# Kernel optimization log

Hardware: AMD Instinct MI355X
Metric: run time of the kernel (lower is better)

The kernel has to match this reference:

```python
import jax, jax.numpy as jnp
import numpy as np

B, S, E, H = 2, 2048, 1024, 16
HD = E // H

def setup_inputs() -> dict:
    key = jax.random.key(0)
    ks = jax.random.split(key, 12)
    q = jax.random.normal(ks[0], (B, S, E), jnp.float32)
    k = jax.random.normal(ks[1], (B, S, E), jnp.float32)
    v = jax.random.normal(ks[2], (B, S, E), jnp.float32)
    # causal mask: 1.0 where attention is disallowed (upper triangle)
    mask = jnp.triu(jnp.ones((S, S), jnp.float32), k=1)[None, None, :, :]
    w = lambda kk: jax.random.normal(kk, (E, E), jnp.float32) * 0.02
    return {
        "q": q, "k": k, "v": v, "mask": mask,
        "Wq": w(ks[3]), "bq": jnp.zeros((E,), jnp.float32),
        "Wk": w(ks[4]), "bk": jnp.zeros((E,), jnp.float32),
        "Wv": w(ks[5]), "bv": jnp.zeros((E,), jnp.float32),
        "Wz": w(ks[6]), "bz": jnp.zeros((E,), jnp.float32),
    }

def _create_heads(x):
    # Faithful to tf.reshape(tf.transpose(x), (B, H, -1, HD)):
    # tf.transpose reverses all dims: [B,S,E] -> [E,S,B], then reshape.
    return jnp.transpose(x, (2, 1, 0)).reshape(B, H, -1, HD)

def reference(q, k, v, mask, Wq, bq, Wk, bk, Wv, bv, Wz, bz):
    qh = _create_heads(q @ Wq + bq)  # (B,H,S,HD)
    kh = _create_heads(k @ Wk + bk)
    vh = _create_heads(v @ Wv + bv)
    qn = qh / jnp.linalg.norm(qh, axis=-1, keepdims=True)
    kn = kh / jnp.linalg.norm(kh, axis=-1, keepdims=True)
    logits = jnp.einsum('bhqd,bhkd->bhqk', qn, kn) * 1000.0
    logits = logits + mask * -1000000000.0
    attn = jax.nn.softmax(logits, axis=-1)  # (B,H,S,S)
    z = jnp.einsum('bhqk,bhkd->bhqd', attn, vh)
    zc = jnp.transpose(z, (0, 2, 1, 3)).reshape(B, -1, E)
    return zc @ Wz + bz, attn
```

## Files before the change

kernel.cpp:

```cpp
#include <hip/hip_runtime.h>
#include <cstdint>
#include <cstddef>


typedef __bf16 bf16x4 __attribute__((ext_vector_type(4)));
typedef __bf16 bf16x8 __attribute__((ext_vector_type(8)));
typedef float floatx4 __attribute__((ext_vector_type(4)));

#define GLOAD_LDS16(g, l)                                                      \
    __builtin_amdgcn_global_load_lds(                                          \
        (const __attribute__((address_space(1))) void*)(g),                    \
        (__attribute__((address_space(3))) void*)(l), 16, 0, 0)

__device__ __forceinline__ void nt_store4(float* p, floatx4 v) {
    __builtin_nontemporal_store(v, (floatx4*)p);
}

__global__ __launch_bounds__(256) void prep(
    const float* __restrict__ x0, const float* __restrict__ x1,
    const float* __restrict__ x2, __bf16* __restrict__ ApBase,
    const float* __restrict__ w0, const float* __restrict__ w1,
    const float* __restrict__ w2, const float* __restrict__ w3,
    __bf16* __restrict__ Bp0, __bf16* __restrict__ BpzDst, int nW)
{
    const int flat = (int)blockIdx.x;
    const int tid = (int)threadIdx.x;

    if (flat < 12288) {
        const int z = flat >> 12;
        const int bx = flat & 4095;
        const float* X = z == 0 ? x0 : (z == 1 ? x1 : x2);
        __bf16* Ap = ApBase + (size_t)z * (4096ull * 2048);
        const int idx = bx * 256 + tid;
        const int r = idx >> 8;
        const int c = (idx & 255) * 4;
        float4 t = *(const float4*)(X + (size_t)r * 1024 + c);
        bf16x4 hi, lo;
        hi[0] = (__bf16)t.x; lo[0] = (__bf16)(t.x - (float)hi[0]);
        hi[1] = (__bf16)t.y; lo[1] = (__bf16)(t.y - (float)hi[1]);
        hi[2] = (__bf16)t.z; lo[2] = (__bf16)(t.z - (float)hi[2]);
        hi[3] = (__bf16)t.w; lo[3] = (__bf16)(t.w - (float)hi[3]);
        *(bf16x4*)(Ap + (size_t)r * 2048 + c) = hi;
        *(bf16x4*)(Ap + (size_t)r * 2048 + 1024 + c) = lo;
        return;
    }

    const int t = flat - 12288;
    const int slice = t >> 8;
    if (slice >= nW) return;
    const int idx = t & 255;
    const float* W = slice == 0 ? w0 : (slice == 1 ? w1 : (slice == 2 ? w2 : w3));
    __bf16* Bp = slice < 3 ? (Bp0 + (size_t)slice * (1024ull * 2048)) : BpzDst;

    __shared__ float tile[64][65];
    const int k0 = (idx >> 4) * 64, n0 = (idx & 15) * 64;
    #pragma unroll
    for (int p = 0; p < 4; ++p) {
        int kr = p * 16 + (tid >> 4);
        float4 v = *(const float4*)(W + (size_t)(k0 + kr) * 1024 + n0 + (tid & 15) * 4);
        tile[kr][(tid & 15) * 4 + 0] = v.x; tile[kr][(tid & 15) * 4 + 1] = v.y;
        tile[kr][(tid & 15) * 4 + 2] = v.z; tile[kr][(tid & 15) * 4 + 3] = v.w;
    }
    __syncthreads();
    const int nr = tid >> 2, kc = (tid & 3) * 16;
    bf16x8 hi0, hi1, lo0, lo1;
    #pragma unroll
    for (int j = 0; j < 8; ++j) {
        float x = tile[kc + j][nr];
        __bf16 h = (__bf16)x; hi0[j] = h; lo0[j] = (__bf16)(x - (float)h);
        float y = tile[kc + 8 + j][nr];
        __bf16 g = (__bf16)y; hi1[j] = g; lo1[j] = (__bf16)(y - (float)g);
    }
    __bf16* row = Bp + (size_t)(n0 + nr) * 2048;
    *(bf16x8*)(row + k0 + kc)            = hi0;
    *(bf16x8*)(row + k0 + kc + 8)        = hi1;
    *(bf16x8*)(row + 1024 + k0 + kc)     = lo0;
    *(bf16x8*)(row + 1024 + k0 + kc + 8) = lo1;
}

__global__ __launch_bounds__(256) void split_bt1(
    const float* __restrict__ W, __bf16* __restrict__ Bp)
{
    __shared__ float tile[64][65];
    const int tid = (int)threadIdx.x;
    const int k0 = blockIdx.y * 64, n0 = blockIdx.x * 64;
    #pragma unroll
    for (int p = 0; p < 4; ++p) {
        int kr = p * 16 + (tid >> 4);
        float4 v = *(const float4*)(W + (size_t)(k0 + kr) * 1024 + n0 + (tid & 15) * 4);
        tile[kr][(tid & 15) * 4 + 0] = v.x; tile[kr][(tid & 15) * 4 + 1] = v.y;
        tile[kr][(tid & 15) * 4 + 2] = v.z; tile[kr][(tid & 15) * 4 + 3] = v.w;
    }
    __syncthreads();
    const int nr = tid >> 2, kc = (tid & 3) * 16;
    bf16x8 hi0, hi1, lo0, lo1;
    #pragma unroll
    for (int j = 0; j < 8; ++j) {
        float x = tile[kc + j][nr];
        __bf16 h = (__bf16)x; hi0[j] = h; lo0[j] = (__bf16)(x - (float)h);
        float y = tile[kc + 8 + j][nr];
        __bf16 g = (__bf16)y; hi1[j] = g; lo1[j] = (__bf16)(y - (float)g);
    }
    __bf16* row = Bp + (size_t)(n0 + nr) * 2048;
    *(bf16x8*)(row + k0 + kc)            = hi0;
    *(bf16x8*)(row + k0 + kc + 8)        = hi1;
    *(bf16x8*)(row + 1024 + k0 + kc)     = lo0;
    *(bf16x8*)(row + 1024 + k0 + kc + 8) = lo1;
}

__global__ __launch_bounds__(256) void gemm_split(
    const __bf16* __restrict__ Ap0, size_t aSlice, int aStride,
    const __bf16* __restrict__ Bp0, size_t bSlice,
    const float* __restrict__ b0, const float* __restrict__ b1,
    const float* __restrict__ b2, float* __restrict__ Out0,
    int transposeOut, int chunksQK, int chunksV)
{
    const int z = blockIdx.z;
    const int nch = (z == 2) ? chunksV : chunksQK;
    const __bf16* Ap = Ap0 + (size_t)z * aSlice;
    const __bf16* Bp = Bp0 + (size_t)z * bSlice;
    const float* bias = z == 0 ? b0 : (z == 1 ? b1 : b2);
    float* Out = Out0 + (size_t)z * (4096ull * 1024);

    __shared__ __bf16 As[2 * 128 * 32];
    __shared__ __bf16 Bs[2 * 128 * 32];

    const int tid = (int)threadIdx.x;
    const int wave = tid >> 6, lane = tid & 63;
    const int quad = lane >> 4, tl = lane & 15;
    const int m0 = blockIdx.y * 128, n0 = blockIdx.x * 128;
    const int waveM = wave >> 1, waveN = wave & 1;

    floatx4 acc[4][4];
    #pragma unroll
    for (int i = 0; i < 4; ++i)
        #pragma unroll
        for (int j = 0; j < 4; ++j)
            acc[i][j] = (floatx4){0.f, 0.f, 0.f, 0.f};

    const int sRow  = (wave << 4) + (lane >> 2);
    const int sColB = (lane & 3) << 4;
    auto* AsL = (__attribute__((address_space(3))) char*)As;
    auto* BsL = (__attribute__((address_space(3))) char*)Bs;
    const int ldsOff = wave * 1024;

    for (int k0 = 0; k0 < 1024; k0 += 32) {
        __syncthreads();
        #pragma unroll
        for (int i = 0; i < 2; ++i) {
            GLOAD_LDS16((const char*)(Ap + (size_t)(m0 + i*64 + sRow) * aStride + k0) + sColB,
                        AsL + i * 4096 + ldsOff);
            GLOAD_LDS16((const char*)(Bp + (size_t)(n0 + i*64 + sRow) * 2048 + k0) + sColB,
                        BsL + i * 4096 + ldsOff);
            if (nch > 1) {
                GLOAD_LDS16((const char*)(Ap + 1024 + (size_t)(m0 + i*64 + sRow) * aStride + k0) + sColB,
                            AsL + 8192 + i * 4096 + ldsOff);
                GLOAD_LDS16((const char*)(Bp + 1024 + (size_t)(n0 + i*64 + sRow) * 2048 + k0) + sColB,
                            BsL + 8192 + i * 4096 + ldsOff);
            }
        }
        __syncthreads();

        bf16x8 ah[4], bh[4], al[4], bl[4];
        #pragma unroll
        for (int mt = 0; mt < 4; ++mt)
            ah[mt] = *(const bf16x8*)(As + (waveM*64 + mt*16 + tl) * 32 + quad * 8);
        #pragma unroll
        for (int nt = 0; nt < 4; ++nt)
            bh[nt] = *(const bf16x8*)(Bs + (waveN*64 + nt*16 + tl) * 32 + quad * 8);
        #pragma unroll
        for (int mt = 0; mt < 4; ++mt)
            #pragma unroll
            for (int nt = 0; nt < 4; ++nt)
                acc[mt][nt] = __builtin_amdgcn_mfma_f32_16x16x32_bf16(
                    ah[mt], bh[nt], acc[mt][nt], 0, 0, 0);
        if (nch > 1) {
            #pragma unroll
            for (int mt = 0; mt < 4; ++mt)
                al[mt] = *(const bf16x8*)(As + 4096 + (waveM*64 + mt*16 + tl) * 32 + quad * 8);
            #pragma unroll
            for (int mt = 0; mt < 4; ++mt)
                #pragma unroll
                for (int nt = 0; nt < 4; ++nt)
                    acc[mt][nt] = __builtin_amdgcn_mfma_f32_16x16x32_bf16(
                        al[mt], bh[nt], acc[mt][nt], 0, 0, 0);
        }
        if (nch > 2) {
            #pragma unroll
            for (int nt = 0; nt < 4; ++nt)
                bl[nt] = *(const bf16x8*)(Bs + 4096 + (waveN*64 + nt*16 + tl) * 32 + quad * 8);
            #pragma unroll
            for (int mt = 0; mt < 4; ++mt)
                #pragma unroll
                for (int nt = 0; nt < 4; ++nt)
                    acc[mt][nt] = __builtin_amdgcn_mfma_f32_16x16x32_bf16(
                        ah[mt], bl[nt], acc[mt][nt], 0, 0, 0);
        }
    }

    if (transposeOut) {
        #pragma unroll
        for (int nt = 0; nt < 4; ++nt) {
            const int e = n0 + waveN * 64 + nt * 16 + tl;
            const float bb = bias[e];
            #pragma unroll
            for (int mt = 0; mt < 4; ++mt) {
                floatx4 v = acc[mt][nt] + bb;
                *(floatx4*)(Out + (size_t)e * 4096 + m0 + waveM * 64 + mt * 16 + quad * 4) = v;
            }
        }
    } else {
        #pragma unroll
        for (int mt = 0; mt < 4; ++mt) {
            const int rbase = m0 + waveM * 64 + mt * 16 + quad * 4;
            #pragma unroll
            for (int nt = 0; nt < 4; ++nt) {
                const int e = n0 + waveN * 64 + nt * 16 + tl;
                const float bb = bias[e];
                #pragma unroll
                for (int reg = 0; reg < 4; ++reg)
                    Out[(size_t)(rbase + reg) * 1024 + e] = acc[mt][nt][reg] + bb;
            }
        }
    }
}

__global__ __launch_bounds__(256) void gather_all(
    const float* __restrict__ PT0, __bf16* __restrict__ Qp,
    __bf16* __restrict__ Kp, __bf16* __restrict__ Vt)
{
    const int flat = (int)blockIdx.x;
    const int tid = (int)threadIdx.x;

    if (flat < 32768) {
        const float* PT = flat < 16384 ? PT0 : (PT0 + 4194304);
        __bf16* Outp = flat < 16384 ? Qp : Kp;
        const int bx = flat & 16383;
        const int lane = tid & 63;
        const int vec  = bx * 4 + (tid >> 6);
        const int head = vec >> 11;
        const int sp   = vec & 2047;
        const int c    = (head >> 4) * 512 + (head & 15) * 32 + (sp >> 6);
        const int src  = (lane & 1) * 2048 + (sp & 63) * 32 + (lane >> 1);
        float v = PT[(size_t)c * 4096 + src];
        float ss = v * v;
        #pragma unroll
        for (int mk = 32; mk >= 1; mk >>= 1) ss += __shfl_xor(ss, mk);
        v = v / sqrtf(ss);
        __bf16 h = (__bf16)v;
        Outp[(size_t)vec * 128 + lane]      = h;
        Outp[(size_t)vec * 128 + 64 + lane] = (__bf16)(v - (float)h);
        return;
    }

    const int t = flat - 32768;
    const int st = t & 31, head = t >> 5;
    const float* PTv = PT0 + 8388608;
    const int c = (head >> 4) * 512 + (head & 15) * 32 + st;
    const float* __restrict__ row = PTv + (size_t)c * 4096;

    __shared__ float tile[64][65];
    #pragma unroll
    for (int i = 0; i < 4; ++i) {
        int o = i * 1024 + tid * 4;
        float4 v4 = *(const float4*)(row + o);
        float vals[4] = {v4.x, v4.y, v4.z, v4.w};
        #pragma unroll
        for (int e = 0; e < 4; ++e) {
            int oo = o + e;
            int d  = ((oo & 2047) & 31) * 2 + (oo >> 11);
            int sl = (oo & 2047) >> 5;
            tile[sl][d] = vals[e];
        }
    }
    __syncthreads();

    const int d = tid >> 2, jb = (tid & 3) * 16;
    bf16x8 h0, h1;
    #pragma unroll
    for (int j = 0; j < 8; ++j) {
        h0[j] = (__bf16)tile[jb + j][d];
        h1[j] = (__bf16)tile[jb + 8 + j][d];
    }
    size_t bh = ((size_t)head * 64 + d) * 2048 + st * 64 + jb;
    *(bf16x8*)(Vt + bh)     = h0;
    *(bf16x8*)(Vt + bh + 8) = h1;
}

__global__ __launch_bounds__(512, 4) void attn_mfma(
    const __bf16* __restrict__ Qp, const __bf16* __restrict__ Kp,
    const __bf16* __restrict__ Vt, float* __restrict__ Attn,
    __bf16* __restrict__ Az)
{
    const int flat = (int)blockIdx.x;
    const int head = flat & 31;
    const int idx  = flat >> 5;
    const int it   = (idx < 8) ? (15 - idx) : (idx - 8);
    const int tid = (int)threadIdx.x;
    const int w = tid >> 6, lane = tid & 63;
    const int quad = lane >> 4, tl = lane & 15;
    const int t7 = tl & 7;
    const int i0 = it * 128;
    const int jtmax = 2 * it + 1;
    const int wrowMax = i0 + w * 16 + 15;
    const int wdiag   = (i0 + w * 16) >> 6;
    const int irowBase = w * 16 + quad * 4;

    const __bf16* __restrict__ Qh = Qp + ((size_t)head * 2048 + i0) * 128;
    const __bf16* __restrict__ Kh = Kp + (size_t)head * 2048 * 128;
    const __bf16* __restrict__ Vh = Vt + (size_t)head * 64 * 2048;
    float* __restrict__ Ah = Attn + (size_t)head * ((size_t)2048 * 2048);

    __shared__ __bf16 kb[2][64 * 128];
    __shared__ __bf16 vt[2][64 * 64];
    __shared__ __bf16 ps[8][16 * 72];
    __bf16* psw = ps[w];
    auto* kbL = (__attribute__((address_space(3))) char*)&kb[0][0];
    auto* vtL = (__attribute__((address_space(3))) char*)&vt[0][0];

    const char* kSrc[2];
    #pragma unroll
    for (int i = 0; i < 2; ++i) {
        int d  = i * 512 + tid;
        int rK = d >> 4, cK = (d & 15) ^ (rK & 7);
        kSrc[i] = (const char*)(Kh + (size_t)rK * 128) + cK * 16;
    }
    const char* vSrc;
    {
        int rV = tid >> 3, cV = (tid & 7) ^ (rV & 7);
        vSrc = (const char*)(Vh + (size_t)rV * 2048) + cV * 16;
    }
    const int ok0 = ((quad)      ^ t7) * 8;
    const int ok1 = ((quad + 4)  ^ t7) * 8;
    const int ok2 = ((quad + 8)  ^ t7) * 8;
    const int ok3 = ((quad + 12) ^ t7) * 8;

    const __bf16* qrow = Qh + (size_t)(w * 16 + tl) * 128;
    bf16x8 qhi0 = *(const bf16x8*)(qrow + quad * 8);
    bf16x8 qhi1 = *(const bf16x8*)(qrow + 32 + quad * 8);
    bf16x8 qlo0 = *(const bf16x8*)(qrow + 64 + quad * 8);
    bf16x8 qlo1 = *(const bf16x8*)(qrow + 96 + quad * 8);

    for (int jt = jtmax + 1; jt < 32; ++jt) {
        floatx4 z4 = (floatx4){0.f, 0.f, 0.f, 0.f};
        #pragma unroll
        for (int g = 0; g < 4; ++g)
            nt_store4(Ah + (size_t)(i0 + w * 16 + g * 4 + quad) * 2048
                          + jt * 64 + tl * 4, z4);
    }

    float m[4], l[4];
    #pragma unroll
    for (int r = 0; r < 4; ++r) { m[r] = -3.0e38f; l[r] = 0.0f; }

    #pragma unroll
    for (int i = 0; i < 2; ++i)
        GLOAD_LDS16(kSrc[i], kbL + i * 8192 + w * 1024);

    for (int jt = 0; jt <= jtmax; ++jt) {
        const int cur = jt & 1;
        __syncthreads();
        if (jt < jtmax) {
            #pragma unroll
            for (int i = 0; i < 2; ++i)
                GLOAD_LDS16(kSrc[i] + (size_t)(jt + 1) * 16384,
                            kbL + (cur ^ 1) * 16384 + i * 8192 + w * 1024);
        }
        if (jt * 64 > wrowMax) continue;

        const __bf16* kbuf = &kb[cur][0];
        const bool diag = (jt == wdiag);
        #pragma unroll
        for (int sub = 0; sub < 4; ++sub) {
            const __bf16* kr = kbuf + (sub * 16 + tl) * 128;
            bf16x8 khi0 = *(const bf16x8*)(kr + ok0);
            bf16x8 khi1 = *(const bf16x8*)(kr + ok1);
            bf16x8 klo0 = *(const bf16x8*)(kr + ok2);
            bf16x8 klo1 = *(const bf16x8*)(kr + ok3);
            floatx4 s = (floatx4){0.f, 0.f, 0.f, 0.f};
            s = __builtin_amdgcn_mfma_f32_16x16x32_bf16(qhi0, khi0, s, 0, 0, 0);
            s = __builtin_amdgcn_mfma_f32_16x16x32_bf16(qhi1, khi1, s, 0, 0, 0);
            s = __builtin_amdgcn_mfma_f32_16x16x32_bf16(qhi0, klo0, s, 0, 0, 0);
            s = __builtin_amdgcn_mfma_f32_16x16x32_bf16(qhi1, klo1, s, 0, 0, 0);
            s = __builtin_amdgcn_mfma_f32_16x16x32_bf16(qlo0, khi0, s, 0, 0, 0);
            s = __builtin_amdgcn_mfma_f32_16x16x32_bf16(qlo1, khi1, s, 0, 0, 0);
            const int col = jt * 64 + sub * 16 + tl;
            #pragma unroll
            for (int reg = 0; reg < 4; ++reg) {
                float lv = s[reg] * 1000.0f;
                if (diag && (col > i0 + irowBase + reg)) lv = -1.0e9f;
                float mn = fmaxf(m[reg], lv);
                l[reg] = l[reg] * __expf(m[reg] - mn) + __expf(lv - mn);
                m[reg] = mn;
            }
        }
    }

    #pragma unroll
    for (int reg = 0; reg < 4; ++reg) {
        #pragma unroll
        for (int mk = 8; mk >= 1; mk >>= 1) {
            float mo = __shfl_xor(m[reg], mk);
            float lo = __shfl_xor(l[reg], mk);
            float mn = fmaxf(m[reg], mo);
            l[reg] = l[reg] * __expf(m[reg] - mn) + lo * __expf(mo - mn);
            m[reg] = mn;
        }
    }
    float inv_l[4];
    #pragma unroll
    for (int reg = 0; reg < 4; ++reg) inv_l[reg] = 1.0f / l[reg];

    floatx4 zacc[4];
    #pragma unroll
    for (int t = 0; t < 4; ++t) zacc[t] = (floatx4){0.f, 0.f, 0.f, 0.f};

    #pragma unroll
    for (int i = 0; i < 2; ++i)
        GLOAD_LDS16(kSrc[i], kbL + i * 8192 + w * 1024);
    GLOAD_LDS16(vSrc, vtL + w * 1024);

    for (int jt = 0; jt <= jtmax; ++jt) {
        const int cur = jt & 1;
        __syncthreads();
        if (jt < jtmax) {
            #pragma unroll
            for (int i = 0; i < 2; ++i)
                GLOAD_LDS16(kSrc[i] + (size_t)(jt + 1) * 16384,
                            kbL + (cur ^ 1) * 16384 + i * 8192 + w * 1024);
            GLOAD_LDS16(vSrc + (size_t)(jt + 1) * 128,
                        vtL + (cur ^ 1) * 8192 + w * 1024);
        }

        if (jt * 64 > wrowMax) {
            floatx4 z4 = (floatx4){0.f, 0.f, 0.f, 0.f};
            #pragma unroll
            for (int g = 0; g < 4; ++g)
                nt_store4(Ah + (size_t)(i0 + w * 16 + g * 4 + quad) * 2048
                              + jt * 64 + tl * 4, z4);
            continue;
        }

        const __bf16* kbuf = &kb[cur][0];
        const __bf16* vbuf = &vt[cur][0];
        const bool diag = (jt == wdiag);
        #pragma unroll
        for (int sub = 0; sub < 4; ++sub) {
            const __bf16* kr = kbuf + (sub * 16 + tl) * 128;
            bf16x8 khi0 = *(const bf16x8*)(kr + ok0);
            bf16x8 khi1 = *(const bf16x8*)(kr + ok1);
            bf16x8 klo0 = *(const bf16x8*)(kr + ok2);
            bf16x8 klo1 = *(const bf16x8*)(kr + ok3);
            floatx4 s = (floatx4){0.f, 0.f, 0.f, 0.f};
            s = __builtin_amdgcn_mfma_f32_16x16x32_bf16(qhi0, khi0, s, 0, 0, 0);
            s = __builtin_amdgcn_mfma_f32_16x16x32_bf16(qhi1, khi1, s, 0, 0, 0);
            s = __builtin_amdgcn_mfma_f32_16x16x32_bf16(qhi0, klo0, s, 0, 0, 0);
            s = __builtin_amdgcn_mfma_f32_16x16x32_bf16(qhi1, klo1, s, 0, 0, 0);
            s = __builtin_amdgcn_mfma_f32_16x16x32_bf16(qlo0, khi0, s, 0, 0, 0);
            s = __builtin_amdgcn_mfma_f32_16x16x32_bf16(qlo1, khi1, s, 0, 0, 0);
            const int col = jt * 64 + sub * 16 + tl;
            #pragma unroll
            for (int reg = 0; reg < 4; ++reg) {
                float lv = s[reg] * 1000.0f;
                if (diag && (col > i0 + irowBase + reg)) lv = -1.0e9f;
                float p = __expf(lv - m[reg]) * inv_l[reg];
                psw[(quad * 4 + reg) * 72 + sub * 16 + tl] = (__bf16)p;
            }
        }
        __asm__ volatile("s_waitcnt lgkmcnt(0)" ::: "memory");

        #pragma unroll
        for (int g = 0; g < 4; ++g) {
            bf16x4 pv = *(const bf16x4*)(psw + (g * 4 + quad) * 72 + tl * 4);
            floatx4 f = (floatx4){(float)pv[0], (float)pv[1],
                                  (float)pv[2], (float)pv[3]};
            nt_store4(Ah + (size_t)(i0 + w * 16 + g * 4 + quad) * 2048
                          + jt * 64 + tl * 4, f);
        }

        bf16x8 p0 = *(const bf16x8*)(psw + tl * 72 + quad * 8);
        bf16x8 p1 = *(const bf16x8*)(psw + tl * 72 + 32 + quad * 8);
        #pragma unroll
        for (int t = 0; t < 4; ++t) {
            const __bf16* vh0 = vbuf + (t * 16 + tl) * 64;
            bf16x8 vhi0 = *(const bf16x8*)(vh0 + ok0);
            bf16x8 vhi1 = *(const bf16x8*)(vh0 + ok1);
            zacc[t] = __builtin_amdgcn_mfma_f32_16x16x32_bf16(p0, vhi0, zacc[t], 0, 0, 0);
            zacc[t] = __builtin_amdgcn_mfma_f32_16x16x32_bf16(p1, vhi1, zacc[t], 0, 0, 0);
        }
    }

    const int b = head >> 4, h = head & 15;
    #pragma unroll
    for (int reg = 0; reg < 4; ++reg) {
        const size_t R = (size_t)b * 2048 + i0 + w * 16 + quad * 4 + reg;
        #pragma unroll
        for (int t = 0; t < 4; ++t)
            Az[R * 1024 + h * 64 + t * 16 + tl] = (__bf16)zacc[t][reg];
    }
}

extern "C" void kernel_launch(void* const* d_in, const int* in_sizes, int n_in,
                              void* d_out, int out_size, void* d_ws, size_t ws_size,
                              hipStream_t stream) {
    (void)in_sizes; (void)n_in; (void)out_size;
    const float* q  = (const float*)d_in[0];
    const float* k  = (const float*)d_in[1];
    const float* v  = (const float*)d_in[2];
    const float* Wq = (const float*)d_in[4];  const float* bq = (const float*)d_in[5];
    const float* Wk = (const float*)d_in[6];  const float* bk = (const float*)d_in[7];
    const float* Wv = (const float*)d_in[8];  const float* bv = (const float*)d_in[9];
    const float* Wz = (const float*)d_in[10]; const float* bz = (const float*)d_in[11];

    float* out0 = (float*)d_out;
    float* attn = out0 + 4194304;

    float*  PT0 = attn;
    __bf16* Ap0 = (__bf16*)(attn + 12582912);
    __bf16* Bp0 = (__bf16*)(attn + 12582912 + 12582912);

    __bf16 *Qp, *Kp, *Vtp, *Az, *Bpz;
    const bool bigWs = ws_size >= (size_t)54525952;
    if (bigWs) {
        __bf16* ws = (__bf16*)d_ws;
        Qp = ws; Kp = ws + 8388608; Vtp = ws + 16777216; Az = ws + 20971520;
        Bpz = ws + 25165824;
    } else {
        Qp = (__bf16*)d_in[0]; Kp = (__bf16*)d_in[1]; Vtp = (__bf16*)d_in[2];
        Az = (__bf16*)d_ws;
        Bpz = (__bf16*)d_in[4];
    }

    if (bigWs) {
        prep<<<dim3(12288 + 4 * 256), 256, 0, stream>>>(
            q, k, v, Ap0, Wq, Wk, Wv, Wz, Bp0, Bpz, 4);
    } else {
        prep<<<dim3(12288 + 3 * 256), 256, 0, stream>>>(
            q, k, v, Ap0, Wq, Wk, Wv, Wz, Bp0, nullptr, 3);
        split_bt1<<<dim3(16, 16), 256, 0, stream>>>(Wz, Bpz);
    }

    gemm_split<<<dim3(8, 32, 3), 256, 0, stream>>>(
        Ap0, 4096ull*2048, 2048, Bp0, 1024ull*2048,
        bq, bk, bv, PT0, 1, 3, 1);

    gather_all<<<dim3(33792), 256, 0, stream>>>(PT0, Qp, Kp, Vtp);

    attn_mfma<<<dim3(512), 512, 0, stream>>>(Qp, Kp, Vtp, attn, Az);

    gemm_split<<<dim3(8, 32, 1), 256, 0, stream>>>(
        Az, 0, 1024, Bpz, 0,
        bz, bz, bz, out0, 0, 1, 1);
}
```

Baseline: 806.1 us.

## Fuse Q/K head reshaping and L2 normalization into projection GEMM epilogue

The Q and K projection GEMM blocks now remap their A-row loads so each wave's output tile holds whole head vectors. The epilogue adds bias, computes the L2 norm with a cross-lane shuffle, and writes the normalized hi/lo bf16 split directly into the per-head layout. This removes the fp32 transposed round-trip through PT0 and the separate gather pass for Q and K, leaving a smaller kernel that only transposes V. The cost is scattered 2-byte stores in the epilogue and extra registers in the GEMM.

```diff
diff --git a/kernel.cpp b/kernel.cpp
--- a/kernel.cpp
+++ b/kernel.cpp
@@ -113,10 +113,12 @@
     const __bf16* __restrict__ Bp0, size_t bSlice,
     const float* __restrict__ b0, const float* __restrict__ b1,
     const float* __restrict__ b2, float* __restrict__ Out0,
-    int transposeOut, int chunksQK, int chunksV)
+    int transposeOut, int chunksQK, int chunksV,
+    __bf16* __restrict__ Qp, __bf16* __restrict__ Kp, int fuseQK)
 {
     const int z = blockIdx.z;
     const int nch = (z == 2) ? chunksV : chunksQK;
+    const bool fuse = fuseQK && (z < 2);
     const __bf16* Ap = Ap0 + (size_t)z * aSlice;
     const __bf16* Bp = Bp0 + (size_t)z * bSlice;
     const float* bias = z == 0 ? b0 : (z == 1 ? b1 : b2);
@@ -144,16 +146,28 @@
     auto* BsL = (__attribute__((address_space(3))) char*)Bs;
     const int ldsOff = wave * 1024;
 
+    size_t aRow[2];
+    #pragma unroll
+    for (int i = 0; i < 2; ++i) {
+        const int mrow = i * 64 + sRow;
+        if (fuse) {
+            const int u = mrow & 63;
+            aRow[i] = (size_t)((u >> 5) * 2048 + (m0 >> 1) + (mrow >> 6) * 32 + (u & 31));
+        } else {
+            aRow[i] = (size_t)(m0 + mrow);
+        }
+    }
+
     for (int k0 = 0; k0 < 1024; k0 += 32) {
         __syncthreads();
         #pragma unroll
         for (int i = 0; i < 2; ++i) {
-            GLOAD_LDS16((const char*)(Ap + (size_t)(m0 + i*64 + sRow) * aStride + k0) + sColB,
+            GLOAD_LDS16((const char*)(Ap + aRow[i] * aStride + k0) + sColB,
                         AsL + i * 4096 + ldsOff);
             GLOAD_LDS16((const char*)(Bp + (size_t)(n0 + i*64 + sRow) * 2048 + k0) + sColB,
                         BsL + i * 4096 + ldsOff);
             if (nch > 1) {
-                GLOAD_LDS16((const char*)(Ap + 1024 + (size_t)(m0 + i*64 + sRow) * aStride + k0) + sColB,
+                GLOAD_LDS16((const char*)(Ap + 1024 + aRow[i] * aStride + k0) + sColB,
                             AsL + 8192 + i * 4096 + ldsOff);
                 GLOAD_LDS16((const char*)(Bp + 1024 + (size_t)(n0 + i*64 + sRow) * 2048 + k0) + sColB,
                             BsL + 8192 + i * 4096 + ldsOff);
@@ -198,7 +212,42 @@
         }
     }
 
-    if (transposeOut) {
+    if (fuse) {
+        __bf16* Outp = (z == 0) ? Qp : Kp;
+        const int g = ((m0 >> 7) << 1) + waveM;
+        #pragma unroll
+        for (int nt = 0; nt < 4; ++nt) {
+            const int e = n0 + waveN * 64 + nt * 16 + tl;
+            const float bb = bias[e];
+            float vals[16];
+            float ss = 0.f;
+            #pragma unroll
+            for (int mt = 0; mt < 4; ++mt)
+                #pragma unroll
+                for (int reg = 0; reg < 4; ++reg) {
+                    float vv = acc[mt][nt][reg] + bb;
+                    vals[mt * 4 + reg] = vv;
+                    ss += vv * vv;
+                }
+            ss += __shfl_xor(ss, 16);
+            ss += __shfl_xor(ss, 32);
+            const float inv = 1.0f / sqrtf(ss);
+            const int head = ((e >> 9) << 4) + ((e >> 5) & 15);
+            const int sp = ((e & 31) << 6) + g;
+            __bf16* row = Outp + ((size_t)head * 2048 + sp) * 128;
+            #pragma unroll
+            for (int mt = 0; mt < 4; ++mt)
+                #pragma unroll
+                for (int reg = 0; reg < 4; ++reg) {
+                    const int u = mt * 16 + quad * 4 + reg;
+                    const int d = ((u & 31) << 1) | (u >> 5);
+                    float vv = vals[mt * 4 + reg] * inv;
+                    __bf16 h = (__bf16)vv;
+                    row[d] = h;
+                    row[64 + d] = (__bf16)(vv - (float)h);
+                }
+        }
+    } else if (transposeOut) {
         #pragma unroll
         for (int nt = 0; nt < 4; ++nt) {
             const int e = n0 + waveN * 64 + nt * 16 + tl;
@@ -225,35 +274,11 @@
     }
 }
 
-__global__ __launch_bounds__(256) void gather_all(
-    const float* __restrict__ PT0, __bf16* __restrict__ Qp,
-    __bf16* __restrict__ Kp, __bf16* __restrict__ Vt)
+__global__ __launch_bounds__(256) void v_transpose(
+    const float* __restrict__ PT0, __bf16* __restrict__ Vt)
 {
-    const int flat = (int)blockIdx.x;
+    const int t = (int)blockIdx.x;
     const int tid = (int)threadIdx.x;
-
-    if (flat < 32768) {
-        const float* PT = flat < 16384 ? PT0 : (PT0 + 4194304);
-        __bf16* Outp = flat < 16384 ? Qp : Kp;
-        const int bx = flat & 16383;
-        const int lane = tid & 63;
-        const int vec  = bx * 4 + (tid >> 6);
-        const int head = vec >> 11;
-        const int sp   = vec & 2047;
-        const int c    = (head >> 4) * 512 + (head & 15) * 32 + (sp >> 6);
-        const int src  = (lane & 1) * 2048 + (sp & 63) * 32 + (lane >> 1);
-        float v = PT[(size_t)c * 4096 + src];
-        float ss = v * v;
-        #pragma unroll
-        for (int mk = 32; mk >= 1; mk >>= 1) ss += __shfl_xor(ss, mk);
-        v = v / sqrtf(ss);
-        __bf16 h = (__bf16)v;
-        Outp[(size_t)vec * 128 + lane]      = h;
-        Outp[(size_t)vec * 128 + 64 + lane] = (__bf16)(v - (float)h);
-        return;
-    }
-
-    const int t = flat - 32768;
     const int st = t & 31, head = t >> 5;
     const float* PTv = PT0 + 8388608;
     const int c = (head >> 4) * 512 + (head & 15) * 32 + st;
@@ -542,13 +567,15 @@
 
     gemm_split<<<dim3(8, 32, 3), 256, 0, stream>>>(
         Ap0, 4096ull*2048, 2048, Bp0, 1024ull*2048,
-        bq, bk, bv, PT0, 1, 3, 1);
-
-    gather_all<<<dim3(33792), 256, 0, stream>>>(PT0, Qp, Kp, Vtp);
+        bq, bk, bv, PT0, 1, 3, 1,
+        Qp, Kp, 1);
+
+    v_transpose<<<dim3(1024), 256, 0, stream>>>(PT0, Vtp);
 
     attn_mfma<<<dim3(512), 512, 0, stream>>>(Qp, Kp, Vtp, attn, Az);
 
     gemm_split<<<dim3(8, 32, 1), 256, 0, stream>>>(
         Az, 0, 1024, Bpz, 0,
-        bz, bz, bz, out0, 0, 1, 1);
-}
+        bz, bz, bz, out0, 0, 1, 1,
+        nullptr, nullptr, 0);
+}
```

Result: no change. 807.6 us (+0.2%).
